# Kernel tuning notes

Measured on AMD Instinct MI355X. Metric: run time of the kernel, lower is better.

## Reference

```python
import jax, jax.numpy as jnp
import numpy as np

N_NODES = 50000
N_EDGES = 1_600_000
D = 64        # node/edge feature dim
RBF = 9       # radial basis degree
DIN = 3 * D   # concat(vi, vj, e)


def _gated_mlp(x, l1w, l1b, l2w, l2b, g1w, g1b, g2w, g2b):
    # layers branch: SiLU on every layer (activate_last=True)
    h = jax.nn.silu(x @ l1w.T + l1b)
    h = jax.nn.silu(h @ l2w.T + l2b)
    # gates branch: SiLU on hidden, sigmoid on last
    g = jax.nn.silu(x @ g1w.T + g1b)
    g = jax.nn.sigmoid(g @ g2w.T + g2b)
    return h * g


def setup_inputs() -> dict:
    key = jax.random.key(0)
    ks = jax.random.split(key, 24)
    s = 0.05
    inp = {
        "node_feat": jax.random.normal(ks[0], (N_NODES, D), jnp.float32),
        "edge_feat": jax.random.normal(ks[1], (N_EDGES, D), jnp.float32),
        "rbf": jax.random.normal(ks[2], (N_EDGES, RBF), jnp.float32),
        "src": jax.random.randint(ks[3], (N_EDGES,), 0, N_NODES, jnp.int32),
        "dst": jax.random.randint(ks[4], (N_EDGES,), 0, N_NODES, jnp.int32),
        # edge GatedMLP params
        "e_l1_w": jax.random.normal(ks[5], (D, DIN)) * s,  "e_l1_b": jnp.zeros((D,)),
        "e_l2_w": jax.random.normal(ks[6], (D, D)) * s,    "e_l2_b": jnp.zeros((D,)),
        "e_g1_w": jax.random.normal(ks[7], (D, DIN)) * s,  "e_g1_b": jnp.zeros((D,)),
        "e_g2_w": jax.random.normal(ks[8], (D, D)) * s,    "e_g2_b": jnp.zeros((D,)),
        # node GatedMLP params
        "n_l1_w": jax.random.normal(ks[9], (D, DIN)) * s,  "n_l1_b": jnp.zeros((D,)),
        "n_l2_w": jax.random.normal(ks[10], (D, D)) * s,   "n_l2_b": jnp.zeros((D,)),
        "n_g1_w": jax.random.normal(ks[11], (D, DIN)) * s, "n_g1_b": jnp.zeros((D,)),
        "n_g2_w": jax.random.normal(ks[12], (D, D)) * s,   "n_g2_b": jnp.zeros((D,)),
        # rbf -> weight linear projections (bias=False)
        "edge_w_w": jax.random.normal(ks[13], (D, RBF)) * s,
        "node_w_w": jax.random.normal(ks[14], (D, RBF)) * s,
    }
    return inp


def reference(node_feat, edge_feat, rbf, src, dst,
              e_l1_w, e_l1_b, e_l2_w, e_l2_b, e_g1_w, e_g1_b, e_g2_w, e_g2_b,
              n_l1_w, n_l1_b, n_l2_w, n_l2_b, n_g1_w, n_g1_b, n_g2_w, n_g2_b,
              edge_w_w, node_w_w):
    vi = node_feat[src]   # [E, D] gather src node features
    vj = node_feat[dst]   # [E, D] gather dst node features

    # ---- edge update: GatedMLP(concat) * Linear(rbf) ----
    x_e = jnp.concatenate([vi, vj, edge_feat], axis=1)  # [E, 3D]
    edge_update = _gated_mlp(x_e, e_l1_w, e_l1_b, e_l2_w, e_l2_b,
                             e_g1_w, e_g1_b, e_g2_w, e_g2_b) * (rbf @ edge_w_w.T)
    e_new = edge_feat + edge_update

    # ---- node update: per-edge message then scatter-sum to dst ----
    x_n = jnp.concatenate([vi, vj, e_new], axis=1)  # uses updated edge features
    mess = _gated_mlp(x_n, n_l1_w, n_l1_b, n_l2_w, n_l2_b,
                      n_g1_w, n_g1_b, n_g2_w, n_g2_b) * (rbf @ node_w_w.T)
    ve = jax.ops.segment_sum(mess, dst, num_segments=N_NODES)  # [N, D]
    v_new = node_feat + ve

    return e_new, v_new
```

## Files before the change

### kernel.cpp

```cpp
#include <hip/hip_runtime.h>

#define TILE_E 128

typedef __attribute__((ext_vector_type(8))) short bf16x8;
typedef __attribute__((ext_vector_type(4))) float f32x4;

__device__ __forceinline__ unsigned int f2bf(float f) {
    union { float f; unsigned int u; } v; v.f = f;
    return (v.u + 0x7FFFu + ((v.u >> 16) & 1u)) >> 16;
}
__device__ __forceinline__ unsigned int cvt_pk_bf16(float lo, float hi) {
    unsigned int r;
    asm("v_cvt_pk_bf16_f32 %0, %1, %2" : "=v"(r) : "v"(lo), "v"(hi));
    return r;
}
__device__ __forceinline__ float fsigmoid(float x) { return 1.0f / (1.0f + __expf(-x)); }
__device__ __forceinline__ float fsilu(float x) { return x * fsigmoid(x); }

#define O_EL1 0
#define O_EG1 12288
#define O_EL2 24576
#define O_EG2 28672
#define O_NL1 32768
#define O_NG1 45056
#define O_NL2 57344
#define O_NG2 61440

__global__ void prep_weights(const float* el1, const float* eg1, const float* el2, const float* eg2,
                             const float* nl1, const float* ng1, const float* nl2, const float* ng2,
                             unsigned short* wout) {
    int tid = blockIdx.x * 256 + threadIdx.x;
    if (tid >= 65536) return;
    int idx = tid; const float* s; int base, K;
    if (idx < 12288)      { s = el1; base = O_EL1; K = 192; }
    else if (idx < 24576) { idx -= 12288; s = eg1; base = O_EG1; K = 192; }
    else if (idx < 28672) { idx -= 24576; s = el2; base = O_EL2; K = 64; }
    else if (idx < 32768) { idx -= 28672; s = eg2; base = O_EG2; K = 64; }
    else if (idx < 45056) { idx -= 32768; s = nl1; base = O_NL1; K = 192; }
    else if (idx < 57344) { idx -= 45056; s = ng1; base = O_NG1; K = 192; }
    else if (idx < 61440) { idx -= 57344; s = nl2; base = O_NL2; K = 64; }
    else                  { idx -= 61440; s = ng2; base = O_NG2; K = 64; }
    int n = (K == 192) ? (idx / 192) : (idx >> 6);
    int k = idx - n * K;
    int off = (((n >> 4) * (K >> 5) + (k >> 5)) * 4 + ((k >> 3) & 3)) * 128 + ((n & 15) << 3) + (k & 7);
    wout[base + off] = (unsigned short)f2bf(s[idx]);
}

__global__ void vinit(const float* __restrict__ node_feat, float* __restrict__ out_v, int n) {
    int i = blockIdx.x * 256 + threadIdx.x;
    if (i < n) out_v[i] = node_feat[i];
}

__device__ __forceinline__ int xswz(int c) { return c ^ ((c >> 4) & 7); }
__device__ __forceinline__ int hswz(int c) { return c ^ ((c >> 3) & 7); }

template<bool ISX>
__device__ __forceinline__ void store_hidden(unsigned short* __restrict__ base, int lane,
                                             const f32x4 acc[4], const float b[4]) {
    const int qp = lane >> 4, ln = lane & 15;
    #pragma unroll
    for (int nt = 0; nt < 4; ++nt) {
        const int f = nt * 16 + ln;
        const int cb = ((f >> 5) * 4 + ((f >> 3) & 3)) * 16 + qp * 4;
        const int j2 = f & 7;
        unsigned int p0 = cvt_pk_bf16(fsilu(acc[nt][0] + b[nt]), fsilu(acc[nt][1] + b[nt]));
        unsigned int p1 = cvt_pk_bf16(fsilu(acc[nt][2] + b[nt]), fsilu(acc[nt][3] + b[nt]));
        const int c0 = ISX ? (256 + xswz(cb + 0)) : hswz(cb + 0);
        const int c1 = ISX ? (256 + xswz(cb + 1)) : hswz(cb + 1);
        const int c2 = ISX ? (256 + xswz(cb + 2)) : hswz(cb + 2);
        const int c3 = ISX ? (256 + xswz(cb + 3)) : hswz(cb + 3);
        base[c0 * 8 + j2] = (unsigned short)p0;
        base[c1 * 8 + j2] = (unsigned short)(p0 >> 16);
        base[c2 * 8 + j2] = (unsigned short)p1;
        base[c3 * 8 + j2] = (unsigned short)(p1 >> 16);
    }
}

__device__ __forceinline__ void gated_mlp(
    unsigned short* __restrict__ Xw, unsigned short* __restrict__ Hw,
    const unsigned short* __restrict__ wb,
    int oL1, int oL2, int oG1, int oG2,
    const float* __restrict__ bL1, const float* __restrict__ bL2,
    const float* __restrict__ bG1, const float* __restrict__ bG2,
    int lane, f32x4 prod[4])
{
    const int ln = lane & 15;

    float b1h[4], b1g[4];
    #pragma unroll
    for (int nt = 0; nt < 4; ++nt) { b1h[nt] = bL1[nt * 16 + ln]; b1g[nt] = bG1[nt * 16 + ln]; }

    bf16x8 a1[6];
    #pragma unroll
    for (int t = 0; t < 6; ++t)
        a1[t] = *(const bf16x8*)(Xw + xswz(t * 64 + lane) * 8);

    f32x4 acc[4];
    #pragma unroll
    for (int nt = 0; nt < 4; ++nt) acc[nt] = (f32x4){0.f, 0.f, 0.f, 0.f};
    #pragma unroll
    for (int nt = 0; nt < 4; ++nt)
        #pragma unroll
        for (int t = 0; t < 6; ++t) {
            bf16x8 bfr = *(const bf16x8*)(wb + oL1 + (nt * 6 + t) * 512 + lane * 8);
            acc[nt] = __builtin_amdgcn_mfma_f32_16x16x32_bf16(a1[t], bfr, acc[nt], 0, 0, 0);
        }
    store_hidden<false>(Hw, lane, acc, b1h);

    f32x4 accg[4];
    #pragma unroll
    for (int nt = 0; nt < 4; ++nt) accg[nt] = (f32x4){0.f, 0.f, 0.f, 0.f};
    #pragma unroll
    for (int nt = 0; nt < 4; ++nt)
        #pragma unroll
        for (int t = 0; t < 6; ++t) {
            bf16x8 bfr = *(const bf16x8*)(wb + oG1 + (nt * 6 + t) * 512 + lane * 8);
            accg[nt] = __builtin_amdgcn_mfma_f32_16x16x32_bf16(a1[t], bfr, accg[nt], 0, 0, 0);
        }
    store_hidden<true>(Xw, lane, accg, b1g);

    float b2h[4], b2g[4];
    #pragma unroll
    for (int nt = 0; nt < 4; ++nt) { b2h[nt] = bL2[nt * 16 + ln]; b2g[nt] = bG2[nt * 16 + ln]; }

    asm volatile("s_waitcnt lgkmcnt(0)" ::: "memory");

    bf16x8 a2h[2], a2g[2];
    #pragma unroll
    for (int t2 = 0; t2 < 2; ++t2) {
        a2h[t2] = *(const bf16x8*)(Hw + hswz(t2 * 64 + lane) * 8);
        a2g[t2] = *(const bf16x8*)(Xw + (256 + xswz(t2 * 64 + lane)) * 8);
    }

    f32x4 acc2h[4], acc2g[4];
    #pragma unroll
    for (int nt = 0; nt < 4; ++nt) {
        acc2h[nt] = (f32x4){0.f, 0.f, 0.f, 0.f};
        acc2g[nt] = (f32x4){0.f, 0.f, 0.f, 0.f};
    }
    #pragma unroll
    for (int nt = 0; nt < 4; ++nt)
        #pragma unroll
        for (int t2 = 0; t2 < 2; ++t2) {
            bf16x8 bh = *(const bf16x8*)(wb + oL2 + (nt * 2 + t2) * 512 + lane * 8);
            bf16x8 bg = *(const bf16x8*)(wb + oG2 + (nt * 2 + t2) * 512 + lane * 8);
            acc2h[nt] = __builtin_amdgcn_mfma_f32_16x16x32_bf16(a2h[t2], bh, acc2h[nt], 0, 0, 0);
            acc2g[nt] = __builtin_amdgcn_mfma_f32_16x16x32_bf16(a2g[t2], bg, acc2g[nt], 0, 0, 0);
        }

    #pragma unroll
    for (int nt = 0; nt < 4; ++nt)
        #pragma unroll
        for (int r = 0; r < 4; ++r)
            prod[nt][r] = fsilu(acc2h[nt][r] + b2h[nt]) * fsigmoid(acc2g[nt][r] + b2g[nt]);
}

__global__ __launch_bounds__(512, 4) void m3g_main(
    const float* __restrict__ node_feat, const float* __restrict__ edge_feat,
    const float* __restrict__ rbf, const int* __restrict__ src, const int* __restrict__ dst,
    const unsigned short* __restrict__ wb,
    const float* __restrict__ el1b, const float* __restrict__ el2b,
    const float* __restrict__ eg1b, const float* __restrict__ eg2b,
    const float* __restrict__ nl1b, const float* __restrict__ nl2b,
    const float* __restrict__ ng1b, const float* __restrict__ ng2b,
    const float* __restrict__ eww, const float* __restrict__ nww,
    float* __restrict__ out_e, float* __restrict__ out_v, int E)
{
    __shared__ unsigned short Xs[128 * 192];
    __shared__ unsigned short Hs[8 * 1024];

    const int tid = threadIdx.x;
    const int e0 = blockIdx.x * TILE_E;
    const int w = tid >> 6, lane = tid & 63;
    const int qp = lane >> 4, ln = lane & 15;

    {
        const int el = tid >> 2, cb = (tid & 3) * 16;
        const int eg = min(e0 + el, E - 1);
        const int reg = el >> 4;
        const int m = el & 15;
        const float* r0 = node_feat + (size_t)src[eg] * 64;
        const float* r1 = node_feat + (size_t)dst[eg] * 64;
        const float* r2 = edge_feat + (size_t)eg * 64;
        const float* rows[3] = { r0, r1, r2 };
        #pragma unroll
        for (int s = 0; s < 3; ++s) {
            const float4* rp = (const float4*)(rows[s] + cb);
            #pragma unroll
            for (int o = 0; o < 2; ++o) {
                float4 f0 = rp[o * 2], f1 = rp[o * 2 + 1];
                uint4 u;
                u.x = cvt_pk_bf16(f0.x, f0.y);
                u.y = cvt_pk_bf16(f0.z, f0.w);
                u.z = cvt_pk_bf16(f1.x, f1.y);
                u.w = cvt_pk_bf16(f1.z, f1.w);
                int kk = s * 64 + cb + o * 8;
                int chunk = ((kk >> 5) * 4 + ((kk >> 3) & 3)) * 16 + m;
                *(uint4*)&Xs[reg * 3072 + xswz(chunk) * 8] = u;
            }
        }
    }
    __syncthreads();

    unsigned short* Xw = Xs + w * 3072;
    unsigned short* Hw = Hs + w * 1024;

    f32x4 prodE[4];
    gated_mlp(Xw, Hw, wb, O_EL1, O_EL2, O_EG1, O_EG2, el1b, el2b, eg1b, eg2b, lane, prodE);

    {
        float ewv[4][9];
        #pragma unroll
        for (int nt = 0; nt < 4; ++nt)
            #pragma unroll
            for (int ri = 0; ri < 9; ++ri)
                ewv[nt][ri] = eww[(nt * 16 + ln) * 9 + ri];

        #pragma unroll
        for (int r = 0; r < 4; ++r) {
            const int m = qp * 4 + r, el = w * 16 + m, eg = e0 + el;
            if (eg < E) {
                float rb[9];
                #pragma unroll
                for (int ri = 0; ri < 9; ++ri) rb[ri] = rbf[(size_t)eg * 9 + ri];
                #pragma unroll
                for (int nt = 0; nt < 4; ++nt) {
                    float rw = 0.0f;
                    #pragma unroll
                    for (int ri = 0; ri < 9; ++ri) rw += rb[ri] * ewv[nt][ri];
                    const int f = nt * 16 + ln;
                    float en = edge_feat[(size_t)eg * 64 + f] + prodE[nt][r] * rw;
                    out_e[(size_t)eg * 64 + f] = en;
                    const int cE = ((f >> 5) * 4 + ((f >> 3) & 3)) * 16 + m;
                    Xw[(256 + xswz(cE)) * 8 + (f & 7)] = (unsigned short)cvt_pk_bf16(en, en);
                }
            }
        }
    }
    asm volatile("s_waitcnt lgkmcnt(0)" ::: "memory");

    f32x4 prodN[4];
    gated_mlp(Xw, Hw, wb, O_NL1, O_NL2, O_NG1, O_NG2, nl1b, nl2b, ng1b, ng2b, lane, prodN);

    {
        float nwv[4][9];
        #pragma unroll
        for (int nt = 0; nt < 4; ++nt)
            #pragma unroll
            for (int ri = 0; ri < 9; ++ri)
                nwv[nt][ri] = nww[(nt * 16 + ln) * 9 + ri];

        #pragma unroll
        for (int r = 0; r < 4; ++r) {
            const int eg = e0 + w * 16 + qp * 4 + r;
            if (eg < E) {
                float rb[9];
                #pragma unroll
                for (int ri = 0; ri < 9; ++ri) rb[ri] = rbf[(size_t)eg * 9 + ri];
                const int dn = dst[eg];
                #pragma unroll
                for (int nt = 0; nt < 4; ++nt) {
                    float rw = 0.0f;
                    #pragma unroll
                    for (int ri = 0; ri < 9; ++ri) rw += rb[ri] * nwv[nt][ri];
                    unsafeAtomicAdd(&out_v[(size_t)dn * 64 + nt * 16 + ln], prodN[nt][r] * rw);
                }
            }
        }
    }
}

extern "C" void kernel_launch(void* const* d_in, const int* in_sizes, int n_in,
                              void* d_out, int out_size, void* d_ws, size_t ws_size,
                              hipStream_t stream) {
    const float* node_feat = (const float*)d_in[0];
    const float* edge_feat = (const float*)d_in[1];
    const float* rbf  = (const float*)d_in[2];
    const int*   src  = (const int*)d_in[3];
    const int*   dst  = (const int*)d_in[4];
    const float* el1w = (const float*)d_in[5];
    const float* el1b = (const float*)d_in[6];
    const float* el2w = (const float*)d_in[7];
    const float* el2b = (const float*)d_in[8];
    const float* eg1w = (const float*)d_in[9];
    const float* eg1b = (const float*)d_in[10];
    const float* eg2w = (const float*)d_in[11];
    const float* eg2b = (const float*)d_in[12];
    const float* nl1w = (const float*)d_in[13];
    const float* nl1b = (const float*)d_in[14];
    const float* nl2w = (const float*)d_in[15];
    const float* nl2b = (const float*)d_in[16];
    const float* ng1w = (const float*)d_in[17];
    const float* ng1b = (const float*)d_in[18];
    const float* ng2w = (const float*)d_in[19];
    const float* ng2b = (const float*)d_in[20];
    const float* eww  = (const float*)d_in[21];
    const float* nww  = (const float*)d_in[22];

    const int E = in_sizes[1] / 64;
    const int N = in_sizes[0] / 64;
    float* out_e = (float*)d_out;
    float* out_v = out_e + (size_t)E * 64;
    unsigned short* wbf = (unsigned short*)d_ws;

    prep_weights<<<256, 256, 0, stream>>>(el1w, eg1w, el2w, eg2w, nl1w, ng1w, nl2w, ng2w, wbf);
    vinit<<<(N * 64 + 255) / 256, 256, 0, stream>>>(node_feat, out_v, N * 64);
    m3g_main<<<(E + TILE_E - 1) / TILE_E, 512, 0, stream>>>(
        node_feat, edge_feat, rbf, src, dst, wbf,
        el1b, el2b, eg1b, eg2b, nl1b, nl2b, ng1b, ng2b,
        eww, nww, out_e, out_v, E);
}
```

Baseline: 1.657 ms.

## Drop hidden LDS buffer, keep node operands in registers, raise occupancy

The separate per-wave hidden buffer is removed. Both hidden activations are now written into the already-consumed vi/vj part of each wave's X tile, which cuts shared memory per block from about 64KB to about 48KB. The launch bound goes from 4 to 6 so more blocks can fit per CU. The vi/vj A-fragments stay in registers across both gated MLPs, so only the updated edge chunks are reloaded, and dst indices are cached in LDS. The rbf projection weights are read per use instead of being held in register arrays. The aim is higher occupancy to hide gather and atomic latency, at the risk of register pressure or spills under the tighter bound.

```diff
diff --git a/kernel.cpp b/kernel.cpp
--- a/kernel.cpp
+++ b/kernel.cpp
@@ -54,7 +54,6 @@
 __device__ __forceinline__ int xswz(int c) { return c ^ ((c >> 4) & 7); }
 __device__ __forceinline__ int hswz(int c) { return c ^ ((c >> 3) & 7); }
 
-template<bool ISX>
 __device__ __forceinline__ void store_hidden(unsigned short* __restrict__ base, int lane,
                                              const f32x4 acc[4], const float b[4]) {
     const int qp = lane >> 4, ln = lane & 15;
@@ -65,35 +64,26 @@
         const int j2 = f & 7;
         unsigned int p0 = cvt_pk_bf16(fsilu(acc[nt][0] + b[nt]), fsilu(acc[nt][1] + b[nt]));
         unsigned int p1 = cvt_pk_bf16(fsilu(acc[nt][2] + b[nt]), fsilu(acc[nt][3] + b[nt]));
-        const int c0 = ISX ? (256 + xswz(cb + 0)) : hswz(cb + 0);
-        const int c1 = ISX ? (256 + xswz(cb + 1)) : hswz(cb + 1);
-        const int c2 = ISX ? (256 + xswz(cb + 2)) : hswz(cb + 2);
-        const int c3 = ISX ? (256 + xswz(cb + 3)) : hswz(cb + 3);
-        base[c0 * 8 + j2] = (unsigned short)p0;
-        base[c1 * 8 + j2] = (unsigned short)(p0 >> 16);
-        base[c2 * 8 + j2] = (unsigned short)p1;
-        base[c3 * 8 + j2] = (unsigned short)(p1 >> 16);
+        base[hswz(cb + 0) * 8 + j2] = (unsigned short)p0;
+        base[hswz(cb + 1) * 8 + j2] = (unsigned short)(p0 >> 16);
+        base[hswz(cb + 2) * 8 + j2] = (unsigned short)p1;
+        base[hswz(cb + 3) * 8 + j2] = (unsigned short)(p1 >> 16);
     }
 }
 
 __device__ __forceinline__ void gated_mlp(
-    unsigned short* __restrict__ Xw, unsigned short* __restrict__ Hw,
+    unsigned short* __restrict__ Xw,
     const unsigned short* __restrict__ wb,
     int oL1, int oL2, int oG1, int oG2,
     const float* __restrict__ bL1, const float* __restrict__ bL2,
     const float* __restrict__ bG1, const float* __restrict__ bG2,
-    int lane, f32x4 prod[4])
+    int lane, const bf16x8 a1[6], f32x4 prod[4])
 {
     const int ln = lane & 15;
 
     float b1h[4], b1g[4];
     #pragma unroll
     for (int nt = 0; nt < 4; ++nt) { b1h[nt] = bL1[nt * 16 + ln]; b1g[nt] = bG1[nt * 16 + ln]; }
-
-    bf16x8 a1[6];
-    #pragma unroll
-    for (int t = 0; t < 6; ++t)
-        a1[t] = *(const bf16x8*)(Xw + xswz(t * 64 + lane) * 8);
 
     f32x4 acc[4];
     #pragma unroll
@@ -105,7 +95,7 @@
             bf16x8 bfr = *(const bf16x8*)(wb + oL1 + (nt * 6 + t) * 512 + lane * 8);
             acc[nt] = __builtin_amdgcn_mfma_f32_16x16x32_bf16(a1[t], bfr, acc[nt], 0, 0, 0);
         }
-    store_hidden<false>(Hw, lane, acc, b1h);
+    store_hidden(Xw, lane, acc, b1h);
 
     f32x4 accg[4];
     #pragma unroll
@@ -117,7 +107,7 @@
             bf16x8 bfr = *(const bf16x8*)(wb + oG1 + (nt * 6 + t) * 512 + lane * 8);
             accg[nt] = __builtin_amdgcn_mfma_f32_16x16x32_bf16(a1[t], bfr, accg[nt], 0, 0, 0);
         }
-    store_hidden<true>(Xw, lane, accg, b1g);
+    store_hidden(Xw + 1024, lane, accg, b1g);
 
     float b2h[4], b2g[4];
     #pragma unroll
@@ -128,8 +118,8 @@
     bf16x8 a2h[2], a2g[2];
     #pragma unroll
     for (int t2 = 0; t2 < 2; ++t2) {
-        a2h[t2] = *(const bf16x8*)(Hw + hswz(t2 * 64 + lane) * 8);
-        a2g[t2] = *(const bf16x8*)(Xw + (256 + xswz(t2 * 64 + lane)) * 8);
+        a2h[t2] = *(const bf16x8*)(Xw + hswz(t2 * 64 + lane) * 8);
+        a2g[t2] = *(const bf16x8*)(Xw + 1024 + hswz(t2 * 64 + lane) * 8);
     }
 
     f32x4 acc2h[4], acc2g[4];
@@ -155,7 +145,7 @@
             prod[nt][r] = fsilu(acc2h[nt][r] + b2h[nt]) * fsigmoid(acc2g[nt][r] + b2g[nt]);
 }
 
-__global__ __launch_bounds__(512, 4) void m3g_main(
+__global__ __launch_bounds__(512, 6) void m3g_main(
     const float* __restrict__ node_feat, const float* __restrict__ edge_feat,
     const float* __restrict__ rbf, const int* __restrict__ src, const int* __restrict__ dst,
     const unsigned short* __restrict__ wb,
@@ -167,12 +157,14 @@
     float* __restrict__ out_e, float* __restrict__ out_v, int E)
 {
     __shared__ unsigned short Xs[128 * 192];
-    __shared__ unsigned short Hs[8 * 1024];
+    __shared__ int dsts[128];
 
     const int tid = threadIdx.x;
     const int e0 = blockIdx.x * TILE_E;
     const int w = tid >> 6, lane = tid & 63;
     const int qp = lane >> 4, ln = lane & 15;
+
+    if (tid < 128) { int eg = e0 + tid; dsts[tid] = (eg < E) ? dst[eg] : 0; }
 
     {
         const int el = tid >> 2, cb = (tid & 3) * 16;
@@ -203,68 +195,58 @@
     __syncthreads();
 
     unsigned short* Xw = Xs + w * 3072;
-    unsigned short* Hw = Hs + w * 1024;
+
+    bf16x8 a1[6];
+    #pragma unroll
+    for (int t = 0; t < 6; ++t)
+        a1[t] = *(const bf16x8*)(Xw + xswz(t * 64 + lane) * 8);
 
     f32x4 prodE[4];
-    gated_mlp(Xw, Hw, wb, O_EL1, O_EL2, O_EG1, O_EG2, el1b, el2b, eg1b, eg2b, lane, prodE);
-
-    {
-        float ewv[4][9];
-        #pragma unroll
-        for (int nt = 0; nt < 4; ++nt)
-            #pragma unroll
-            for (int ri = 0; ri < 9; ++ri)
-                ewv[nt][ri] = eww[(nt * 16 + ln) * 9 + ri];
-
-        #pragma unroll
-        for (int r = 0; r < 4; ++r) {
-            const int m = qp * 4 + r, el = w * 16 + m, eg = e0 + el;
-            if (eg < E) {
-                float rb[9];
+    gated_mlp(Xw, wb, O_EL1, O_EL2, O_EG1, O_EG2, el1b, el2b, eg1b, eg2b, lane, a1, prodE);
+
+    #pragma unroll
+    for (int r = 0; r < 4; ++r) {
+        const int m = qp * 4 + r, el = w * 16 + m, eg = e0 + el;
+        if (eg < E) {
+            float rb[9];
+            #pragma unroll
+            for (int ri = 0; ri < 9; ++ri) rb[ri] = rbf[(size_t)eg * 9 + ri];
+            #pragma unroll
+            for (int nt = 0; nt < 4; ++nt) {
+                const int f = nt * 16 + ln;
+                float rw = 0.0f;
                 #pragma unroll
-                for (int ri = 0; ri < 9; ++ri) rb[ri] = rbf[(size_t)eg * 9 + ri];
+                for (int ri = 0; ri < 9; ++ri) rw += rb[ri] * eww[f * 9 + ri];
+                float en = edge_feat[(size_t)eg * 64 + f] + prodE[nt][r] * rw;
+                out_e[(size_t)eg * 64 + f] = en;
+                const int cE = ((f >> 5) * 4 + ((f >> 3) & 3)) * 16 + m;
+                Xw[(256 + xswz(cE)) * 8 + (f & 7)] = (unsigned short)cvt_pk_bf16(en, en);
+            }
+        }
+    }
+    asm volatile("s_waitcnt lgkmcnt(0)" ::: "memory");
+
+    a1[4] = *(const bf16x8*)(Xw + xswz(4 * 64 + lane) * 8);
+    a1[5] = *(const bf16x8*)(Xw + xswz(5 * 64 + lane) * 8);
+
+    f32x4 prodN[4];
+    gated_mlp(Xw, wb, O_NL1, O_NL2, O_NG1, O_NG2, nl1b, nl2b, ng1b, ng2b, lane, a1, prodN);
+
+    #pragma unroll
+    for (int r = 0; r < 4; ++r) {
+        const int el = w * 16 + qp * 4 + r, eg = e0 + el;
+        if (eg < E) {
+            float rb[9];
+            #pragma unroll
+            for (int ri = 0; ri < 9; ++ri) rb[ri] = rbf[(size_t)eg * 9 + ri];
+            const int dn = dsts[el];
+            #pragma unroll
+            for (int nt = 0; nt < 4; ++nt) {
+                const int f = nt * 16 + ln;
+                float rw = 0.0f;
                 #pragma unroll
-                for (int nt = 0; nt < 4; ++nt) {
-                    float rw = 0.0f;
-                    #pragma unroll
-                    for (int ri = 0; ri < 9; ++ri) rw += rb[ri] * ewv[nt][ri];
-                    const int f = nt * 16 + ln;
-                    float en = edge_feat[(size_t)eg * 64 + f] + prodE[nt][r] * rw;
-                    out_e[(size_t)eg * 64 + f] = en;
-                    const int cE = ((f >> 5) * 4 + ((f >> 3) & 3)) * 16 + m;
-                    Xw[(256 + xswz(cE)) * 8 + (f & 7)] = (unsigned short)cvt_pk_bf16(en, en);
-                }
-            }
-        }
-    }
-    asm volatile("s_waitcnt lgkmcnt(0)" ::: "memory");
-
-    f32x4 prodN[4];
-    gated_mlp(Xw, Hw, wb, O_NL1, O_NL2, O_NG1, O_NG2, nl1b, nl2b, ng1b, ng2b, lane, prodN);
-
-    {
-        float nwv[4][9];
-        #pragma unroll
-        for (int nt = 0; nt < 4; ++nt)
-            #pragma unroll
-            for (int ri = 0; ri < 9; ++ri)
-                nwv[nt][ri] = nww[(nt * 16 + ln) * 9 + ri];
-
-        #pragma unroll
-        for (int r = 0; r < 4; ++r) {
-            const int eg = e0 + w * 16 + qp * 4 + r;
-            if (eg < E) {
-                float rb[9];
-                #pragma unroll
-                for (int ri = 0; ri < 9; ++ri) rb[ri] = rbf[(size_t)eg * 9 + ri];
-                const int dn = dst[eg];
-                #pragma unroll
-                for (int nt = 0; nt < 4; ++nt) {
-                    float rw = 0.0f;
-                    #pragma unroll
-                    for (int ri = 0; ri < 9; ++ri) rw += rb[ri] * nwv[nt][ri];
-                    unsafeAtomicAdd(&out_v[(size_t)dn * 64 + nt * 16 + ln], prodN[nt][r] * rw);
-                }
+                for (int ri = 0; ri < 9; ++ri) rw += rb[ri] * nww[f * 9 + ri];
+                unsafeAtomicAdd(&out_v[(size_t)dn * 64 + f], prodN[nt][r] * rw);
             }
         }
     }
```

After: 2.024 ms. 22.2% more time.
